# Performance work log

Measured on AMD Instinct MI355X. Metric: run time of the kernel, lower is better.

## Reference

```python
import jax, jax.numpy as jnp
import numpy as np
import math

N = 2048       # num_nodes (dense graph)
F_IN = 256     # num_in_features
F_OUT = 256    # num_out_features
H = 8          # num_heads
LN_EPS = 1e-5

# NOTE: every e3nn FullyConnectedTensorProduct in this module maps
# (Fx0e) x irreps_sh -> (Kx0e). Only the l=0 spherical-harmonic component can
# couple scalars to scalars, and Y_0 = 1 under normalization='component'.
# Each TP is therefore exactly a linear map with a 1/sqrt(fan_in) path norm,
# and edge_direction does not enter the math at all.


def setup_inputs() -> dict:
    key = jax.random.key(0)
    ks = jax.random.split(key, 12)
    inv = 1.0 / np.sqrt(F_IN)
    return {
        "node_features": jax.random.normal(ks[0], (N, F_IN), jnp.float32),
        "edges_features_distance": jax.random.uniform(ks[1], (N, N), jnp.float32),
        "edges_features_bond": jax.random.uniform(ks[2], (N, N), jnp.float32),
        "edge_direction": jax.random.normal(ks[3], (N * N, 3), jnp.float32),
        "degree_matrix": jax.random.randint(ks[4], (N, N), 0, 2).astype(jnp.float32),
        # tensor-product weights (xavier-ish scale)
        "Wq": jax.random.normal(ks[5], (F_IN, H), jnp.float32) * inv,
        "Wk": jax.random.normal(ks[6], (F_IN, H), jnp.float32) * inv,
        "Wv": jax.random.normal(ks[7], (F_IN, F_OUT), jnp.float32) * inv,
        "w_bond": jax.random.normal(ks[8], (), jnp.float32),
        "w_bond_contrib": jax.random.normal(ks[9], (), jnp.float32),
        "w_gauss": jax.random.normal(ks[10], (), jnp.float32),
    }


def reference(node_features, edges_features_distance, edges_features_bond,
              edge_direction, degree_matrix, Wq, Wk, Wv,
              w_bond, w_bond_contrib, w_gauss):
    scale = 1.0 / jnp.sqrt(jnp.asarray(F_IN, node_features.dtype))
    # scalar-only tensor products == scaled linears (Y_0 = 1)
    q = (node_features @ Wq) * scale              # [N, H]
    k = (node_features @ Wk) * scale              # [N, H]
    v = (node_features @ Wv) * scale              # [N, F_OUT]

    # raw_attention[i,j,h] = (q_i + k_i)/sqrt(H)  (key.transpose(0,1) picks node i)
    qk = (q + k) / math.sqrt(H)                   # [N, H]
    bond = edges_features_bond * (w_bond * w_bond_contrib)   # [N, N]
    gauss = edges_features_distance * w_gauss                 # [N, N]
    raw = qk[:, None, :] + (bond + gauss)[:, :, None]          # [N, N, H]

    mask = jnp.where(degree_matrix > 0, 0.0, -1e9).astype(raw.dtype)
    scores = jax.nn.leaky_relu(raw, 0.2) + mask[:, :, None]
    # torch F.softmax without dim on a 3-D tensor -> dim=0
    attn = jax.nn.softmax(scores, axis=0)          # [N, N, H]
    # F.dropout treated as identity (eval / deterministic baseline)
    attn_mean = attn.mean(axis=2)                  # [N, N]

    # aggregated[i] = sum_j attn_mean[i,j] * v_j  (value[i,j,:] = v(node_j))
    aggregated = attn_mean @ v                     # [N, F_OUT]
    updated_nodes = jax.nn.elu(aggregated)

    # no_grad connectivity update
    un = jax.lax.stop_gradient(updated_nodes)
    sim = un @ un.T                                # [N, N]
    dd = -jax.lax.stop_gradient(edges_features_distance)
    conn = jax.nn.sigmoid(sim) * dd * jax.lax.stop_gradient(degree_matrix)
    mu = conn.mean(axis=-1, keepdims=True)
    var = conn.var(axis=-1, keepdims=True)
    conn = (conn - mu) * jax.lax.rsqrt(var + LN_EPS)
    conn = conn + conn.T
    return updated_nodes, conn
```

## Files before the change

### kernel.cpp

```cpp
#include <hip/hip_runtime.h>
#include <hip/hip_bf16.h>

#define NN 2048
#define FIN 256
#define FOUT 256
#define HH 8

typedef short bhalf8 __attribute__((ext_vector_type(8)));
typedef float f32x4  __attribute__((ext_vector_type(4)));

__device__ __forceinline__ unsigned short f2b(float f) {
    __hip_bfloat16 h = __float2bfloat16(f);
    return *reinterpret_cast<unsigned short*>(&h);
}
__device__ __forceinline__ float b2f(unsigned short u) {
    __hip_bfloat16 h = *reinterpret_cast<__hip_bfloat16*>(&u);
    return __bfloat162float(h);
}

__global__ __launch_bounds__(256) void k1_qkv(
    const float* __restrict__ x, const float* __restrict__ Wq,
    const float* __restrict__ Wk, const float* __restrict__ Wv,
    unsigned short* __restrict__ vtb, float* __restrict__ qk,
    float* __restrict__ D8, float* __restrict__ rowsum, float* __restrict__ rowsq)
{
    const int ib = blockIdx.x * 4;
    const int t  = threadIdx.x;
    {
        const int tp = blockIdx.x*256 + t;
        D8[tp] = 0.f;
        if      (tp < 2048) rowsum[tp] = 0.f;
        else if (tp < 4096) rowsq[tp - 2048] = 0.f;
    }
    __shared__ float xs[4][FIN];
    __shared__ float part[256];
    #pragma unroll
    for (int n = 0; n < 4; ++n) xs[n][t] = x[(long)(ib+n)*FIN + t];
    __syncthreads();
    float a0 = 0.f, a1 = 0.f, a2 = 0.f, a3 = 0.f;
    #pragma unroll 4
    for (int c = 0; c < FIN; ++c) {
        const float wv = Wv[c*FOUT + t];
        a0 = fmaf(xs[0][c], wv, a0); a1 = fmaf(xs[1][c], wv, a1);
        a2 = fmaf(xs[2][c], wv, a2); a3 = fmaf(xs[3][c], wv, a3);
    }
    ushort4 uv;
    uv.x = f2b(a0 * 0.0625f); uv.y = f2b(a1 * 0.0625f);
    uv.z = f2b(a2 * 0.0625f); uv.w = f2b(a3 * 0.0625f);
    *(ushort4*)&vtb[(long)t*NN + ib] = uv;
    {
        const int n = t >> 6, h = t & 7, seg = (t >> 3) & 7;
        float a = 0.f;
        for (int c = seg*32; c < seg*32 + 32; ++c)
            a = fmaf(xs[n][c], Wq[c*HH + h] + Wk[c*HH + h], a);
        part[t] = a;
    }
    __syncthreads();
    if (t < 32) {
        const int n = t >> 3, h = t & 7;
        float a = 0.f;
        #pragma unroll
        for (int s2 = 0; s2 < 8; ++s2) a += part[n*64 + s2*8 + h];
        qk[(ib+n)*HH + h] = a * (0.0625f * 0.35355339059327373f);
    }
}

__global__ __launch_bounds__(256) void k2_denom(
    const float* __restrict__ bond, const float* __restrict__ dist,
    const float* __restrict__ deg, const float* __restrict__ qk,
    const float* __restrict__ wb, const float* __restrict__ wbc,
    const float* __restrict__ wg, float* __restrict__ D8,
    unsigned short* __restrict__ fbuf, unsigned short* __restrict__ ddb)
{
    const float cb = wb[0] * wbc[0];
    const float cg = wg[0];
    const int t  = threadIdx.x;
    const int tx = t & 63;
    const int ty = t >> 6;
    const int j0 = blockIdx.x * 256;
    const int i0 = blockIdx.y * 32;
    const int j  = j0 + tx*4;
    __shared__ float qs[32*8];
    __shared__ float red[4][2048];
    for (int p = t; p < 256; p += 256) qs[p] = qk[i0*8 + p];
    __syncthreads();
    float acc[4][8];
    #pragma unroll
    for (int jj = 0; jj < 4; ++jj)
        #pragma unroll
        for (int h = 0; h < 8; ++h) acc[jj][h] = 0.f;
    const int ibase = i0 + ty*8;
    #pragma unroll
    for (int ii = 0; ii < 8; ++ii) {
        const long idx = (long)(ibase + ii)*NN + j;
        const float4 dv = *(const float4*)&dist[idx];
        const float4 bv = *(const float4*)&bond[idx];
        const float4 gv = *(const float4*)&deg[idx];
        ushort4 fb, db;
        fb.x = f2b((gv.x > 0.f) ? fmaf(cb, bv.x, cg*dv.x) : -__builtin_inff());
        fb.y = f2b((gv.y > 0.f) ? fmaf(cb, bv.y, cg*dv.y) : -__builtin_inff());
        fb.z = f2b((gv.z > 0.f) ? fmaf(cb, bv.z, cg*dv.z) : -__builtin_inff());
        fb.w = f2b((gv.w > 0.f) ? fmaf(cb, bv.w, cg*dv.w) : -__builtin_inff());
        db.x = f2b(-dv.x * gv.x); db.y = f2b(-dv.y * gv.y);
        db.z = f2b(-dv.z * gv.z); db.w = f2b(-dv.w * gv.w);
        *(ushort4*)&fbuf[idx] = fb;
        *(ushort4*)&ddb[idx]  = db;
        float s[4];
        s[0] = b2f(fb.x); s[1] = b2f(fb.y); s[2] = b2f(fb.z); s[3] = b2f(fb.w);
        const float* qrow = &qs[(ty*8 + ii)*8];
        #pragma unroll
        for (int h = 0; h < 8; ++h) {
            const float q = qrow[h];
            #pragma unroll
            for (int jj = 0; jj < 4; ++jj) {
                float r = q + s[jj];
                r = fmaxf(r, 0.2f*r);
                acc[jj][h] += __expf(r);
            }
        }
    }
    #pragma unroll
    for (int jj = 0; jj < 4; ++jj)
        #pragma unroll
        for (int h = 0; h < 8; ++h) red[ty][(tx*4 + jj)*8 + h] = acc[jj][h];
    __syncthreads();
    const int bucket = (blockIdx.y & 7) << 14;
    for (int p = t; p < 2048; p += 256) {
        const float ssum = red[0][p] + red[1][p] + red[2][p] + red[3][p];
        atomicAdd(&D8[bucket + j0*8 + p], ssum);
    }
}

__global__ __launch_bounds__(256) void k3_attnmean(
    const unsigned short* __restrict__ fbuf, const float* __restrict__ qk,
    const float* __restrict__ D8, unsigned short* __restrict__ amb)
{
    const int t  = threadIdx.x;
    const int tx = t & 63;
    const int ty = t >> 6;
    const int j0 = blockIdx.x * 256;
    const int i0 = blockIdx.y * 32;
    const int j  = j0 + tx*4;
    __shared__ float qs[32*8];
    __shared__ float Dred[2048];
    for (int p = t; p < 256; p += 256) qs[p] = qk[i0*8 + p];
    for (int p = t; p < 2048; p += 256) {
        float s = 0.f;
        #pragma unroll
        for (int o = 0; o < 8; ++o) s += D8[(o << 14) + j0*8 + p];
        Dred[p] = 0.125f / fmaxf(s, 1e-30f);
    }
    __syncthreads();
    float invD[4][8];
    #pragma unroll
    for (int jj = 0; jj < 4; ++jj)
        #pragma unroll
        for (int h = 0; h < 8; ++h)
            invD[jj][h] = Dred[(tx*4 + jj)*8 + h];
    const int ibase = i0 + ty*8;
    #pragma unroll
    for (int ii = 0; ii < 8; ++ii) {
        const long idx = (long)(ibase + ii)*NN + j;
        const ushort4 fb = *(const ushort4*)&fbuf[idx];
        float s[4];
        s[0] = b2f(fb.x); s[1] = b2f(fb.y); s[2] = b2f(fb.z); s[3] = b2f(fb.w);
        float o[4] = {0.f, 0.f, 0.f, 0.f};
        const float* qrow = &qs[(ty*8 + ii)*8];
        #pragma unroll
        for (int h = 0; h < 8; ++h) {
            const float q = qrow[h];
            #pragma unroll
            for (int jj = 0; jj < 4; ++jj) {
                float r = q + s[jj];
                r = fmaxf(r, 0.2f*r);
                o[jj] = fmaf(__expf(r), invD[jj][h], o[jj]);
            }
        }
        ushort4 ob;
        ob.x = f2b(o[0]); ob.y = f2b(o[1]); ob.z = f2b(o[2]); ob.w = f2b(o[3]);
        *(ushort4*)&amb[idx] = ob;
    }
}

__global__ __launch_bounds__(256) void k4_aggr(
    const unsigned short* __restrict__ amb,
    const unsigned short* __restrict__ vtb,
    float* __restrict__ out0, unsigned short* __restrict__ unb)
{
    const int w = threadIdx.x >> 6, lane = threadIdx.x & 63;
    const int vw = blockIdx.x*4 + w;
    const int it = vw >> 3;
    const int f0 = (vw & 7) * 32;
    const int lm = lane & 15, lq = lane >> 4;
    const unsigned short* arow  = &amb[(long)(it*16 + lm)*NN + lq*8];
    const unsigned short* brow0 = &vtb[(long)(f0 + lm)*NN + lq*8];
    const unsigned short* brow1 = &vtb[(long)(f0 + 16 + lm)*NN + lq*8];
    f32x4 acc0 = {0.f, 0.f, 0.f, 0.f};
    f32x4 acc1 = {0.f, 0.f, 0.f, 0.f};
    #pragma unroll 4
    for (int kk = 0; kk < NN; kk += 32) {
        const bhalf8 a  = *(const bhalf8*)&arow[kk];
        const bhalf8 b0 = *(const bhalf8*)&brow0[kk];
        const bhalf8 b1 = *(const bhalf8*)&brow1[kk];
        acc0 = __builtin_amdgcn_mfma_f32_16x16x32_bf16(a, b0, acc0, 0, 0, 0);
        acc1 = __builtin_amdgcn_mfma_f32_16x16x32_bf16(a, b1, acc1, 0, 0, 0);
    }
    #pragma unroll
    for (int r = 0; r < 4; ++r) {
        const int i = it*16 + lq*4 + r;
        float s0 = acc0[r], s1 = acc1[r];
        s0 = (s0 > 0.f) ? s0 : (__expf(s0) - 1.f);
        s1 = (s1 > 0.f) ? s1 : (__expf(s1) - 1.f);
        out0[(long)i*FOUT + f0 + lm]      = s0;
        out0[(long)i*FOUT + f0 + 16 + lm] = s1;
        unb [(long)i*FOUT + f0 + lm]      = f2b(s0);
        unb [(long)i*FOUT + f0 + 16 + lm] = f2b(s1);
    }
}

__global__ __launch_bounds__(256) void k5_sim(
    const unsigned short* __restrict__ unb, const unsigned short* __restrict__ ddb,
    unsigned short* __restrict__ c0,
    float* __restrict__ rowsum, float* __restrict__ rowsq)
{
    const int i0 = blockIdx.y * 64;
    const int j0 = blockIdx.x * 64;
    const int w  = threadIdx.x >> 6;
    const int l  = threadIdx.x & 63;
    const int lm = l & 15, lq = l >> 4;
    const int iw = i0 + w*16;
    f32x4 acc[4] = {f32x4{0,0,0,0}, f32x4{0,0,0,0}, f32x4{0,0,0,0}, f32x4{0,0,0,0}};
    for (int kk = 0; kk < FOUT; kk += 32) {
        const bhalf8 a = *(const bhalf8*)&unb[(long)(iw + lm)*FOUT + kk + lq*8];
        #pragma unroll
        for (int c = 0; c < 4; ++c) {
            const bhalf8 b = *(const bhalf8*)&unb[(long)(j0 + c*16 + lm)*FOUT + kk + lq*8];
            acc[c] = __builtin_amdgcn_mfma_f32_16x16x32_bf16(a, b, acc[c], 0, 0, 0);
        }
    }
    float srow[4] = {0.f,0.f,0.f,0.f}, qrow[4] = {0.f,0.f,0.f,0.f};
    #pragma unroll
    for (int c = 0; c < 4; ++c) {
        #pragma unroll
        for (int r = 0; r < 4; ++r) {
            const int i = iw + lq*4 + r;
            const int j = j0 + c*16 + lm;
            const long idx = (long)i*NN + j;
            const float sg = 1.f / (1.f + __expf(-acc[c][r]));
            const float val = sg * b2f(ddb[idx]);
            c0[idx] = f2b(val);
            srow[r] += val;
            qrow[r] = fmaf(val, val, qrow[r]);
        }
    }
    #pragma unroll
    for (int r = 0; r < 4; ++r) {
        #pragma unroll
        for (int m = 8; m >= 1; m >>= 1) {
            srow[r] += __shfl_xor(srow[r], m, 64);
            qrow[r] += __shfl_xor(qrow[r], m, 64);
        }
        if (lm == 0) {
            atomicAdd(&rowsum[iw + lq*4 + r], srow[r]);
            atomicAdd(&rowsq [iw + lq*4 + r], qrow[r]);
        }
    }
}

__global__ __launch_bounds__(256) void k7_conn(
    const unsigned short* __restrict__ c0, const float* __restrict__ rowsum,
    const float* __restrict__ rowsq, float* __restrict__ out1)
{
    const int i0 = blockIdx.y * 64;
    const int j0 = blockIdx.x * 64;
    const int t  = threadIdx.x;
    __shared__ float LT[64][68];
    __shared__ float mui[64], rii[64], muj[64], rsj[64];
    const int r  = t >> 4;
    const int c4 = (t & 15) * 4;
    if (t < 64) {
        const float m = rowsum[j0 + t] * (1.f/NN);
        muj[t] = m;
        rsj[t] = rsqrtf(rowsq[j0 + t]*(1.f/NN) - m*m + 1e-5f);
    } else if (t < 128) {
        const int rr = t - 64;
        const float m = rowsum[i0 + rr] * (1.f/NN);
        mui[rr] = m;
        rii[rr] = rsqrtf(rowsq[i0 + rr]*(1.f/NN) - m*m + 1e-5f);
    }
    #pragma unroll
    for (int p = 0; p < 4; ++p) {
        const int jl = r + p*16;
        const ushort4 q = *(const ushort4*)&c0[(long)(j0 + jl)*NN + i0 + c4];
        LT[c4+0][jl] = b2f(q.x); LT[c4+1][jl] = b2f(q.y);
        LT[c4+2][jl] = b2f(q.z); LT[c4+3][jl] = b2f(q.w);
    }
    __syncthreads();
    #pragma unroll
    for (int p = 0; p < 4; ++p) {
        const int rr = r + p*16;
        const int i  = i0 + rr;
        const ushort4 xb = *(const ushort4*)&c0[(long)i*NN + j0 + c4];
        const float mi = mui[rr], ri = rii[rr];
        float4 o;
        o.x = (b2f(xb.x) - mi)*ri + (LT[rr][c4+0] - muj[c4+0])*rsj[c4+0];
        o.y = (b2f(xb.y) - mi)*ri + (LT[rr][c4+1] - muj[c4+1])*rsj[c4+1];
        o.z = (b2f(xb.z) - mi)*ri + (LT[rr][c4+2] - muj[c4+2])*rsj[c4+2];
        o.w = (b2f(xb.w) - mi)*ri + (LT[rr][c4+3] - muj[c4+3])*rsj[c4+3];
        *(float4*)&out1[(long)i*NN + j0 + c4] = o;
    }
}

extern "C" void kernel_launch(void* const* d_in, const int* in_sizes, int n_in,
                              void* d_out, int out_size, void* d_ws, size_t ws_size,
                              hipStream_t stream)
{
    const float* x    = (const float*)d_in[0];
    const float* dist = (const float*)d_in[1];
    const float* bond = (const float*)d_in[2];
    const float* deg  = (const float*)d_in[4];
    const float* Wq   = (const float*)d_in[5];
    const float* Wk   = (const float*)d_in[6];
    const float* Wv   = (const float*)d_in[7];
    const float* wb   = (const float*)d_in[8];
    const float* wbc  = (const float*)d_in[9];
    const float* wg   = (const float*)d_in[10];

    float* out0 = (float*)d_out;
    float* out1 = out0 + (size_t)NN*FOUT;

    char* w = (char*)d_ws;
    unsigned short* fbuf_c0 = (unsigned short*)(w);
    unsigned short* amb  = (unsigned short*)(w +  8388608);
    unsigned short* ddb  = (unsigned short*)(w + 16777216);
    unsigned short* vtb  = (unsigned short*)(w + 25165824);
    unsigned short* unb  = (unsigned short*)(w + 26214400);
    float* qk      = (float*)(w + 27262976);
    float* D8      = (float*)(w + 27328512);
    float* rowsum  = (float*)(w + 27852800);
    float* rowsq   = (float*)(w + 27860992);

    k1_qkv<<<NN/4, 256, 0, stream>>>(x, Wq, Wk, Wv, vtb, qk, D8, rowsum, rowsq);
    dim3 g23(NN/256, NN/32);
    k2_denom<<<g23, 256, 0, stream>>>(bond, dist, deg, qk, wb, wbc, wg, D8, fbuf_c0, ddb);
    k3_attnmean<<<g23, 256, 0, stream>>>(fbuf_c0, qk, D8, amb);
    k4_aggr<<<NN/8, 256, 0, stream>>>(amb, vtb, out0, unb);
    dim3 g5(NN/64, NN/64);
    k5_sim<<<g5, 256, 0, stream>>>(unb, ddb, fbuf_c0, rowsum, rowsq);
    k7_conn<<<g5, 256, 0, stream>>>(fbuf_c0, rowsum, rowsq, out1);
}
```

Baseline: 236.0 us.

## Remap denominator and attention-mean kernels to wave-local tiles with shuffle reductions

k2_denom and k3_attnmean now give each wave a 64-column by 16-row tile, with lanes split into 4 row groups of 16 column groups. The column sums in k2 are reduced with cross-lane shuffles instead of the shared-memory `red` array and barrier. The q values are read straight from global memory rather than staged in LDS, and k3 stores the inverse denominators head-major. Rows per block halve, so the grid doubles. This cuts LDS use and syncs and should raise occupancy, at the cost of twice as many D8 atomics and shorter contiguous row segments per load.

Result: slower. 301.0 us (+27.6%).

```diff
diff --git a/kernel.cpp b/kernel.cpp
--- a/kernel.cpp
+++ b/kernel.cpp
@@ -74,25 +74,22 @@
 {
     const float cb = wb[0] * wbc[0];
     const float cg = wg[0];
-    const int t  = threadIdx.x;
-    const int tx = t & 63;
-    const int ty = t >> 6;
+    const int t    = threadIdx.x;
+    const int wave = t >> 6, lane = t & 63;
+    const int lq   = lane >> 4;
+    const int lj   = lane & 15;
     const int j0 = blockIdx.x * 256;
-    const int i0 = blockIdx.y * 32;
-    const int j  = j0 + tx*4;
-    __shared__ float qs[32*8];
-    __shared__ float red[4][2048];
-    for (int p = t; p < 256; p += 256) qs[p] = qk[i0*8 + p];
-    __syncthreads();
+    const int i0 = blockIdx.y * 16;
+    const int j  = j0 + wave*64 + lj*4;
     float acc[4][8];
     #pragma unroll
     for (int jj = 0; jj < 4; ++jj)
         #pragma unroll
         for (int h = 0; h < 8; ++h) acc[jj][h] = 0.f;
-    const int ibase = i0 + ty*8;
-    #pragma unroll
-    for (int ii = 0; ii < 8; ++ii) {
-        const long idx = (long)(ibase + ii)*NN + j;
+    #pragma unroll
+    for (int ii = 0; ii < 4; ++ii) {
+        const int i = i0 + lq*4 + ii;
+        const long idx = (long)i*NN + j;
         const float4 dv = *(const float4*)&dist[idx];
         const float4 bv = *(const float4*)&bond[idx];
         const float4 gv = *(const float4*)&deg[idx];
@@ -107,10 +104,12 @@
         *(ushort4*)&ddb[idx]  = db;
         float s[4];
         s[0] = b2f(fb.x); s[1] = b2f(fb.y); s[2] = b2f(fb.z); s[3] = b2f(fb.w);
-        const float* qrow = &qs[(ty*8 + ii)*8];
+        const float4 q0 = *(const float4*)&qk[i*8];
+        const float4 q1 = *(const float4*)&qk[i*8 + 4];
+        const float qh[8] = {q0.x, q0.y, q0.z, q0.w, q1.x, q1.y, q1.z, q1.w};
         #pragma unroll
         for (int h = 0; h < 8; ++h) {
-            const float q = qrow[h];
+            const float q = qh[h];
             #pragma unroll
             for (int jj = 0; jj < 4; ++jj) {
                 float r = q + s[jj];
@@ -122,12 +121,18 @@
     #pragma unroll
     for (int jj = 0; jj < 4; ++jj)
         #pragma unroll
-        for (int h = 0; h < 8; ++h) red[ty][(tx*4 + jj)*8 + h] = acc[jj][h];
-    __syncthreads();
+        for (int h = 0; h < 8; ++h) {
+            float v = acc[jj][h];
+            v += __shfl_xor(v, 16, 64);
+            v += __shfl_xor(v, 32, 64);
+            acc[jj][h] = v;
+        }
     const int bucket = (blockIdx.y & 7) << 14;
-    for (int p = t; p < 2048; p += 256) {
-        const float ssum = red[0][p] + red[1][p] + red[2][p] + red[3][p];
-        atomicAdd(&D8[bucket + j0*8 + p], ssum);
+    #pragma unroll
+    for (int h = 0; h < 8; ++h) {
+        const float a = (lq == 0) ? acc[0][h] : (lq == 1) ? acc[1][h]
+                       : (lq == 2) ? acc[2][h] : acc[3][h];
+        atomicAdd(&D8[bucket + (j + lq)*8 + h], a);
     }
 }
 
@@ -135,20 +140,20 @@
     const unsigned short* __restrict__ fbuf, const float* __restrict__ qk,
     const float* __restrict__ D8, unsigned short* __restrict__ amb)
 {
-    const int t  = threadIdx.x;
-    const int tx = t & 63;
-    const int ty = t >> 6;
+    const int t    = threadIdx.x;
+    const int wave = t >> 6, lane = t & 63;
+    const int lq   = lane >> 4;
+    const int lj   = lane & 15;
     const int j0 = blockIdx.x * 256;
-    const int i0 = blockIdx.y * 32;
-    const int j  = j0 + tx*4;
-    __shared__ float qs[32*8];
-    __shared__ float Dred[2048];
-    for (int p = t; p < 256; p += 256) qs[p] = qk[i0*8 + p];
+    const int i0 = blockIdx.y * 16;
+    const int j  = j0 + wave*64 + lj*4;
+    __shared__ float DredT[8][256];
     for (int p = t; p < 2048; p += 256) {
+        const int h = p >> 8, jl = p & 255;
         float s = 0.f;
         #pragma unroll
-        for (int o = 0; o < 8; ++o) s += D8[(o << 14) + j0*8 + p];
-        Dred[p] = 0.125f / fmaxf(s, 1e-30f);
+        for (int o = 0; o < 8; ++o) s += D8[(o << 14) + (j0 + jl)*8 + h];
+        DredT[h][jl] = 0.125f / fmaxf(s, 1e-30f);
     }
     __syncthreads();
     float invD[4][8];
@@ -156,19 +161,21 @@
     for (int jj = 0; jj < 4; ++jj)
         #pragma unroll
         for (int h = 0; h < 8; ++h)
-            invD[jj][h] = Dred[(tx*4 + jj)*8 + h];
-    const int ibase = i0 + ty*8;
-    #pragma unroll
-    for (int ii = 0; ii < 8; ++ii) {
-        const long idx = (long)(ibase + ii)*NN + j;
+            invD[jj][h] = DredT[h][wave*64 + lj*4 + jj];
+    #pragma unroll
+    for (int ii = 0; ii < 4; ++ii) {
+        const int i = i0 + lq*4 + ii;
+        const long idx = (long)i*NN + j;
         const ushort4 fb = *(const ushort4*)&fbuf[idx];
         float s[4];
         s[0] = b2f(fb.x); s[1] = b2f(fb.y); s[2] = b2f(fb.z); s[3] = b2f(fb.w);
         float o[4] = {0.f, 0.f, 0.f, 0.f};
-        const float* qrow = &qs[(ty*8 + ii)*8];
+        const float4 q0 = *(const float4*)&qk[i*8];
+        const float4 q1 = *(const float4*)&qk[i*8 + 4];
+        const float qh[8] = {q0.x, q0.y, q0.z, q0.w, q1.x, q1.y, q1.z, q1.w};
         #pragma unroll
         for (int h = 0; h < 8; ++h) {
-            const float q = qrow[h];
+            const float q = qh[h];
             #pragma unroll
             for (int jj = 0; jj < 4; ++jj) {
                 float r = q + s[jj];
@@ -341,7 +348,7 @@
     float* rowsq   = (float*)(w + 27860992);
 
     k1_qkv<<<NN/4, 256, 0, stream>>>(x, Wq, Wk, Wv, vtb, qk, D8, rowsum, rowsq);
-    dim3 g23(NN/256, NN/32);
+    dim3 g23(NN/256, NN/16);
     k2_denom<<<g23, 256, 0, stream>>>(bond, dist, deg, qk, wb, wbc, wg, D8, fbuf_c0, ddb);
     k3_attnmean<<<g23, 256, 0, stream>>>(fbuf_c0, qk, D8, amb);
     k4_aggr<<<NN/8, 256, 0, stream>>>(amb, vtb, out0, unb);
```
